# Kernel optimization log

Measured on AMD Instinct MI355X. Metric: run time of the kernel, lower is better.

## Reference

```python
import jax, jax.numpy as jnp
import numpy as np

N_HEADS = 16
MAX_LEN = 4096
D_MODEL = 1024
EPS = 1e-6


def setup_inputs() -> dict:
    key = jax.random.key(0)
    ks = jax.random.split(key, 12)
    B, L, D = 4, 4096, D_MODEL
    s = 1.0 / np.sqrt(D)
    inp = {
        "q": jax.random.normal(ks[0], (B, L, D), jnp.float32),
        "k": jax.random.normal(ks[1], (B, L, D), jnp.float32),
        "v": jax.random.normal(ks[2], (B, L, D), jnp.float32),
        "Wq": jax.random.normal(ks[3], (D, D), jnp.float32) * s,
        "bq": jax.random.normal(ks[4], (D,), jnp.float32) * s,
        "Wk": jax.random.normal(ks[5], (D, D), jnp.float32) * s,
        "bk": jax.random.normal(ks[6], (D,), jnp.float32) * s,
        "Wv": jax.random.normal(ks[7], (D, D), jnp.float32) * s,
        "bv": jax.random.normal(ks[8], (D,), jnp.float32) * s,
        "Wo": jax.random.normal(ks[9], (D, D), jnp.float32) * s,
        "bo": jax.random.normal(ks[10], (D,), jnp.float32) * s,
    }
    return inp


def _cos_attn(q, k, v, Wq, bq, Wk, bk, Wv, bv, Wo, bo):
    B, Lq, D = q.shape
    Lk = k.shape[1]
    H = N_HEADS
    hd = D // H
    # torch Linear: x @ W^T + b
    qh = (q @ Wq.T + bq).reshape(B, Lq, H, hd).transpose(0, 2, 1, 3)  # b h l d
    kh = (k @ Wk.T + bk).reshape(B, Lk, H, hd).transpose(0, 2, 1, 3)
    vh = (v @ Wv.T + bv).reshape(B, Lk, H, hd).transpose(0, 2, 1, 3)
    qh = jax.nn.relu(qh)
    kh = jax.nn.relu(kh)
    # weight_index buffer: pi*(1..max_len)/(2*max_len), shape (1,1,L,1)
    idx = (np.pi * jnp.arange(1, MAX_LEN + 1, dtype=jnp.float32) / (2 * MAX_LEN))
    qi = idx[:Lq][None, None, :, None]
    ki = idx[:Lk][None, None, :, None]
    q_ = jnp.concatenate([qh * jnp.sin(qi), qh * jnp.cos(qi)], axis=-1)  # b h l 2d
    k_ = jnp.concatenate([kh * jnp.sin(ki), kh * jnp.cos(ki)], axis=-1)
    kv_ = jnp.einsum("bnld,bnlm->bndm", k_, vh)  # b h 2d d
    z_ = 1.0 / jnp.maximum(jnp.einsum("bnld,bnd->bnl", q_, jnp.sum(k_, axis=2)), EPS)
    attn = jnp.einsum("bnld,bndm,bnl->bnlm", q_, kv_, z_)  # b h l d
    attn = attn.transpose(0, 2, 1, 3).reshape(B, Lq, D)
    return attn @ Wo.T + bo  # dropout: eval mode (identity)


def reference(q, k, v, Wq, bq, Wk, bk, Wv, bv, Wo, bo):
    return _cos_attn(q, k, v, Wq, bq, Wk, bk, Wv, bv, Wo, bo)
```

## Files before the change

kernel.cpp:

```cpp
#include <hip/hip_runtime.h>

typedef __bf16 bf16x8 __attribute__((ext_vector_type(8)));
typedef float f32x4 __attribute__((ext_vector_type(4)));

#define PI_F 3.14159265358979323846f

__device__ __forceinline__ unsigned short f2bf(float f) {
  unsigned u = __builtin_bit_cast(unsigned, f);
  u += 0x7fffu + ((u >> 16) & 1u);
  return (unsigned short)(u >> 16);
}

__device__ __forceinline__ unsigned scale_pair(unsigned w, float f) {
  const float lo = __builtin_bit_cast(float, w << 16);
  const float hi = __builtin_bit_cast(float, w & 0xffff0000u);
  return (unsigned)f2bf(lo * f) | ((unsigned)f2bf(hi * f) << 16);
}

#define GLD16(gp, lp)                                          \
  __builtin_amdgcn_global_load_lds(                            \
      (const __attribute__((address_space(1))) void*)(gp),     \
      (__attribute__((address_space(3))) void*)(lp), 16, 0, 0)

struct AReg { float4 a0, a1, a2, a3, a4, a5, a6, a7; };

__device__ __forceinline__ uint4 cvtpk16(float4 x, float4 y) {
  unsigned c0, c1, c2, c3;
  asm("v_cvt_pk_bf16_f32 %0, %1, %2" : "=v"(c0) : "v"(x.x), "v"(x.y));
  asm("v_cvt_pk_bf16_f32 %0, %1, %2" : "=v"(c1) : "v"(x.z), "v"(x.w));
  asm("v_cvt_pk_bf16_f32 %0, %1, %2" : "=v"(c2) : "v"(y.x), "v"(y.y));
  asm("v_cvt_pk_bf16_f32 %0, %1, %2" : "=v"(c3) : "v"(y.z), "v"(y.w));
  uint4 u; u.x = c0; u.y = c1; u.z = c2; u.w = c3;
  return u;
}

__device__ __forceinline__ uint2 cvtpk8(float a, float b, float c, float d) {
  unsigned lo, hi;
  asm("v_cvt_pk_bf16_f32 %0, %1, %2" : "=v"(lo) : "v"(a), "v"(b));
  asm("v_cvt_pk_bf16_f32 %0, %1, %2" : "=v"(hi) : "v"(c), "v"(d));
  uint2 r; r.x = lo; r.y = hi;
  return r;
}

__device__ __forceinline__ void unpack8(uint4 w, float* f) {
  f[0] = __builtin_bit_cast(float, w.x << 16);
  f[1] = __builtin_bit_cast(float, w.x & 0xffff0000u);
  f[2] = __builtin_bit_cast(float, w.y << 16);
  f[3] = __builtin_bit_cast(float, w.y & 0xffff0000u);
  f[4] = __builtin_bit_cast(float, w.z << 16);
  f[5] = __builtin_bit_cast(float, w.z & 0xffff0000u);
  f[6] = __builtin_bit_cast(float, w.w << 16);
  f[7] = __builtin_bit_cast(float, w.w & 0xffff0000u);
}

__global__ __launch_bounds__(256) void convert_w(
    const float* __restrict__ Wq, const float* __restrict__ Wk,
    const float* __restrict__ Wv, const float* __restrict__ Wo,
    unsigned short* __restrict__ Wqb, unsigned short* __restrict__ Wkb,
    unsigned short* __restrict__ Wvb, unsigned short* __restrict__ Wob) {
  const int region = blockIdx.y;
  const float* s; unsigned short* d;
  switch (region) {
    case 0: s = Wq; d = Wqb; break;
    case 1: s = Wk; d = Wkb; break;
    case 2: s = Wv; d = Wvb; break;
    default: s = Wo; d = Wob; break;
  }
  const float4* s4 = (const float4*)s;
  ushort4* d4 = (ushort4*)d;
  const int n4 = 262144;
  for (int i = blockIdx.x * 256 + threadIdx.x; i < n4; i += gridDim.x * 256) {
    float4 f = s4[i];
    ushort4 o;
    o.x = f2bf(f.x); o.y = f2bf(f.y); o.z = f2bf(f.z); o.w = f2bf(f.w);
    d4[i] = o;
  }
}

template <int MODE>
__global__ __launch_bounds__(512, 2) void gemm256(
    const float* __restrict__ A32, const unsigned short* __restrict__ Bw,
    const float* __restrict__ bias, unsigned short* __restrict__ out) {
  constexpr int K = 1024, NKT = 16;
  __shared__ unsigned short S[65536];
  const int tid = threadIdx.x;
  const int wave = tid >> 6, lane = tid & 63;
  const int fr = lane & 15, fq = lane >> 4;
  const int wr = wave >> 2, wc = wave & 3;
  const int cpx = gridDim.x >> 3;
  const int wg = (blockIdx.x & 7) * cpx + (blockIdx.x >> 3);
  const int mt = wg >> 2, ntile = wg & 3;
  const int m0 = mt * 256, n0 = ntile * 256;

  const int srow = tid >> 3;
  const int ac16 = tid & 7;
  const int scolE = ((ac16 << 4) ^ ((srow & 7) << 4)) >> 1;
  const unsigned short* bSrc = Bw + (size_t)(n0 + srow) * K + scolE;
  const int awoff = (ac16 ^ (srow & 7)) << 3;
  AReg R;

#define BSTAGE(kt_, buf_) do {                                                     \
    const int kc_ = (kt_) * 64;                                                    \
    GLD16(bSrc + kc_,                  S + (buf_) * 32768 + 16384 + wave * 512);   \
    GLD16(bSrc + (size_t)65536 + kc_,  S + (buf_) * 32768 + 20480 + wave * 512);   \
    GLD16(bSrc + (size_t)131072 + kc_, S + (buf_) * 32768 + 24576 + wave * 512);   \
    GLD16(bSrc + (size_t)196608 + kc_, S + (buf_) * 32768 + 28672 + wave * 512);   \
  } while (0)

#define ALOAD_ALL(kt_) do {                                                        \
    const int kc_ = (kt_) * 64;                                                    \
    const float4* p_;                                                              \
    p_ = (const float4*)(A32 + (size_t)(m0 + srow) * K + kc_) + ac16 * 2;          \
    R.a0 = p_[0]; R.a1 = p_[1];                                                    \
    p_ = (const float4*)(A32 + (size_t)(m0 + 64 + srow) * K + kc_) + ac16 * 2;     \
    R.a2 = p_[0]; R.a3 = p_[1];                                                    \
    p_ = (const float4*)(A32 + (size_t)(m0 + 128 + srow) * K + kc_) + ac16 * 2;    \
    R.a4 = p_[0]; R.a5 = p_[1];                                                    \
    p_ = (const float4*)(A32 + (size_t)(m0 + 192 + srow) * K + kc_) + ac16 * 2;    \
    R.a6 = p_[0]; R.a7 = p_[1];                                                    \
  } while (0)

#define AWRITE_ALL(buf_) do {                                                      \
    unsigned short* dst_ = &S[(buf_) * 32768 + srow * 64 + awoff];                 \
    *(uint4*)(dst_)         = cvtpk16(R.a0, R.a1);                                 \
    *(uint4*)(dst_ + 4096)  = cvtpk16(R.a2, R.a3);                                 \
    *(uint4*)(dst_ + 8192)  = cvtpk16(R.a4, R.a5);                                 \
    *(uint4*)(dst_ + 12288) = cvtpk16(R.a6, R.a7);                                 \
  } while (0)

  const int xorv = (fr & 7) << 4;
  const unsigned cbE0 = (unsigned)(((fq * 16) ^ xorv) >> 1);
  const unsigned cbE1 = (unsigned)(((64 + fq * 16) ^ xorv) >> 1);

  f32x4 acc[8][4] = {};
  ALOAD_ALL(0);
  BSTAGE(0, 0);
  AWRITE_ALL(0);
  asm volatile("s_waitcnt vmcnt(0) lgkmcnt(0)" ::: "memory");
  __syncthreads();

  for (int kt = 0; kt < NKT; ++kt) {
    const int buf = kt & 1;
    const unsigned aB = (unsigned)(buf * 32768 + wr * 8192 + fr * 64);
    const unsigned bB = (unsigned)(buf * 32768 + 16384 + (wc >> 1) * 8192 +
                                   ((wc & 1) * 64 + fr) * 64);
    bf16x8 af[4][2], b0[2][2], b1[2][2];
#pragma unroll
    for (int mm = 0; mm < 4; ++mm) {
      const unsigned r = aB + (unsigned)(mm * 1024);
      af[mm][0] = *(const bf16x8*)&S[r + cbE0];
      af[mm][1] = *(const bf16x8*)&S[r + cbE1];
    }
#pragma unroll
    for (int nn = 0; nn < 2; ++nn) {
      const unsigned r0 = bB + (unsigned)(nn * 1024);
      b0[nn][0] = *(const bf16x8*)&S[r0 + cbE0];
      b0[nn][1] = *(const bf16x8*)&S[r0 + cbE1];
      const unsigned r1 = bB + (unsigned)((2 + nn) * 1024);
      b1[nn][0] = *(const bf16x8*)&S[r1 + cbE0];
      b1[nn][1] = *(const bf16x8*)&S[r1 + cbE1];
    }
    if (kt + 1 < NKT) {
      ALOAD_ALL(kt + 1);
      BSTAGE(kt + 1, buf ^ 1);
    }
    __builtin_amdgcn_s_barrier();
    __builtin_amdgcn_s_setprio(1);
#pragma unroll
    for (int mm = 0; mm < 4; ++mm) {
#pragma unroll
      for (int nn = 0; nn < 2; ++nn) {
        acc[mm][nn] = __builtin_amdgcn_mfma_f32_16x16x32_bf16(af[mm][0], b0[nn][0], acc[mm][nn], 0, 0, 0);
        acc[mm][nn] = __builtin_amdgcn_mfma_f32_16x16x32_bf16(af[mm][1], b0[nn][1], acc[mm][nn], 0, 0, 0);
        acc[mm][2 + nn] = __builtin_amdgcn_mfma_f32_16x16x32_bf16(af[mm][0], b1[nn][0], acc[mm][2 + nn], 0, 0, 0);
        acc[mm][2 + nn] = __builtin_amdgcn_mfma_f32_16x16x32_bf16(af[mm][1], b1[nn][1], acc[mm][2 + nn], 0, 0, 0);
      }
    }
    __builtin_amdgcn_s_setprio(0);
    __builtin_amdgcn_s_barrier();
#pragma unroll
    for (int mm = 0; mm < 4; ++mm) {
      const unsigned r = aB + (unsigned)((4 + mm) * 1024);
      af[mm][0] = *(const bf16x8*)&S[r + cbE0];
      af[mm][1] = *(const bf16x8*)&S[r + cbE1];
    }
    if (kt + 1 < NKT) AWRITE_ALL(buf ^ 1);
    __builtin_amdgcn_s_barrier();
    __builtin_amdgcn_s_setprio(1);
#pragma unroll
    for (int mm = 0; mm < 4; ++mm) {
#pragma unroll
      for (int nn = 0; nn < 2; ++nn) {
        acc[4 + mm][nn] = __builtin_amdgcn_mfma_f32_16x16x32_bf16(af[mm][0], b0[nn][0], acc[4 + mm][nn], 0, 0, 0);
        acc[4 + mm][nn] = __builtin_amdgcn_mfma_f32_16x16x32_bf16(af[mm][1], b0[nn][1], acc[4 + mm][nn], 0, 0, 0);
        acc[4 + mm][2 + nn] = __builtin_amdgcn_mfma_f32_16x16x32_bf16(af[mm][0], b1[nn][0], acc[4 + mm][2 + nn], 0, 0, 0);
        acc[4 + mm][2 + nn] = __builtin_amdgcn_mfma_f32_16x16x32_bf16(af[mm][1], b1[nn][1], acc[4 + mm][2 + nn], 0, 0, 0);
      }
    }
    __builtin_amdgcn_s_setprio(0);
    asm volatile("s_waitcnt vmcnt(0) lgkmcnt(0)" ::: "memory");
    __builtin_amdgcn_s_barrier();
  }
#undef BSTAGE
#undef ALOAD_ALL
#undef AWRITE_ALL

  const int colb = n0 + wc * 64 + fr;
  const int rtb0 = wr * 128 + fq * 4;
  const int mlo = m0 & 4095;
  const int b16 = (m0 >> 12) << 4;
  const int hbase = n0 >> 6;

  if constexpr (MODE == 0) {
    float bb4[4];
#pragma unroll
    for (int nq = 0; nq < 4; ++nq) bb4[nq] = bias[colb + nq * 16];
    __syncthreads();
#pragma unroll
    for (int mq = 0; mq < 8; ++mq) {
#pragma unroll
      for (int rr = 0; rr < 4; ++rr) {
        const int rt = rtb0 + mq * 16 + rr;
        const int e = (rt >> 2) & 7;
#pragma unroll
        for (int nq = 0; nq < 4; ++nq) {
          const int ct = wc * 64 + nq * 16 + fr;
          const int sct = (ct & 7) | ((((ct >> 3) ^ e) & 31) << 3);
          S[rt * 256 + sct] = f2bf(fmaxf(acc[mq][nq][rr] + bb4[nq], 0.0f));
        }
      }
    }
    __syncthreads();
#pragma unroll
    for (int it = 0; it < 16; ++it) {
      const int rt = it * 16 + (tid >> 5);
      const int co = tid & 31;
      const int chunk = co ^ ((rt >> 2) & 7);
      uint4 w = *(const uint4*)&S[rt * 256 + chunk * 8];
      const int h = hbase + (co >> 3);
      const size_t addr = ((size_t)(b16 + h) * 4096 + mlo + rt) * 64 + ((co & 7) << 3);
      *(uint4*)(out + addr) = w;
    }
  } else {
    float bb4[4];
#pragma unroll
    for (int nq = 0; nq < 4; ++nq) bb4[nq] = bias[colb + nq * 16];
#pragma unroll
    for (int mq = 0; mq < 8; ++mq)
#pragma unroll
      for (int nq = 0; nq < 4; ++nq)
#pragma unroll
        for (int rr = 0; rr < 4; ++rr) {
          float val = acc[mq][nq][rr] + bb4[nq];
          if constexpr (MODE == 5) val = fmaxf(val, 0.0f);
          acc[mq][nq][rr] = val;
        }
    __syncthreads();
#pragma unroll
    for (int mq = 0; mq < 8; ++mq) {
      const int rtb = rtb0 + mq * 16;
#pragma unroll
      for (int nq = 0; nq < 4; ++nq) {
        const int ct = wc * 64 + nq * 16 + fr;
        uint2 w = cvtpk8(acc[mq][nq][0], acc[mq][nq][1], acc[mq][nq][2], acc[mq][nq][3]);
        *(uint2*)&S[ct * 256 + (rtb ^ ((ct & 7) << 2))] = w;
      }
    }
    __syncthreads();
#pragma unroll
    for (int it = 0; it < 16; ++it) {
      const int ct = it * 16 + (tid >> 5);
      const int lo = (tid & 31) << 3;
      const int sw = (ct & 7) << 2;
      uint2 r0 = *(const uint2*)&S[ct * 256 + (lo ^ sw)];
      uint2 r1 = *(const uint2*)&S[ct * 256 + ((lo + 4) ^ sw)];
      uint4 w; w.x = r0.x; w.y = r0.y; w.z = r1.x; w.w = r1.y;
      const int h = hbase + (ct >> 6), dd = ct & 63;
      const size_t addr = ((size_t)(b16 + h) * 64 + dd) * 4096 + mlo + lo;
      *(uint4*)(out + addr) = w;
    }
  }
}

__global__ __launch_bounds__(512, 2) void gemm_o(
    const unsigned short* __restrict__ Ain, const unsigned short* __restrict__ Bw,
    const float* __restrict__ bias, unsigned short* __restrict__ out) {
  constexpr int K = 1024, NKT = 16;
  __shared__ unsigned short S[65536];
  const int tid = threadIdx.x;
  const int wave = tid >> 6, lane = tid & 63;
  const int fr = lane & 15, fq = lane >> 4;
  const int wr = wave >> 2, wc = wave & 3;
  const int wg = (blockIdx.x & 7) * 32 + (blockIdx.x >> 3);
  const int mt = wg >> 2, ntile = wg & 3;
  const int m0 = mt * 256, n0 = ntile * 256;

  const int srow = tid >> 3;
  const int ac16 = tid & 7;
  const int scolE = ((ac16 << 4) ^ ((srow & 7) << 4)) >> 1;
  const unsigned short* bSrc = Bw + (size_t)(n0 + srow) * K + scolE;
  const unsigned short* aSrcB = Ain + (size_t)(m0 + srow) * K + scolE;

#define BSTAGE(kt_, buf_) do {                                                     \
    const int kc_ = (kt_) * 64;                                                    \
    GLD16(bSrc + kc_,                  S + (buf_) * 32768 + 16384 + wave * 512);   \
    GLD16(bSrc + (size_t)65536 + kc_,  S + (buf_) * 32768 + 20480 + wave * 512);   \
    GLD16(bSrc + (size_t)131072 + kc_, S + (buf_) * 32768 + 24576 + wave * 512);   \
    GLD16(bSrc + (size_t)196608 + kc_, S + (buf_) * 32768 + 28672 + wave * 512);   \
  } while (0)

#define ASTAGE(kt_, buf_) do {                                                     \
    const int kc_ = (kt_) * 64;                                                    \
    GLD16(aSrcB + kc_,                  S + (buf_) * 32768 +     0 + wave * 512);  \
    GLD16(aSrcB + (size_t)65536 + kc_,  S + (buf_) * 32768 +  4096 + wave * 512);  \
    GLD16(aSrcB + (size_t)131072 + kc_, S + (buf_) * 32768 +  8192 + wave * 512);  \
    GLD16(aSrcB + (size_t)196608 + kc_, S + (buf_) * 32768 + 12288 + wave * 512);  \
  } while (0)

  const int xorv = (fr & 7) << 4;
  const unsigned cbE0 = (unsigned)(((fq * 16) ^ xorv) >> 1);
  const unsigned cbE1 = (unsigned)(((64 + fq * 16) ^ xorv) >> 1);

  f32x4 acc[8][4] = {};
  BSTAGE(0, 0);
  ASTAGE(0, 0);
  asm volatile("s_waitcnt vmcnt(0)" ::: "memory");
  __syncthreads();

  for (int kt = 0; kt < NKT; ++kt) {
    const int buf = kt & 1;
    const unsigned aB = (unsigned)(buf * 32768 + wr * 8192 + fr * 64);
    const unsigned bB = (unsigned)(buf * 32768 + 16384 + (wc >> 1) * 8192 +
                                   ((wc & 1) * 64 + fr) * 64);
    bf16x8 af[4][2], b0[2][2], b1[2][2];
#pragma unroll
    for (int mm = 0; mm < 4; ++mm) {
      const unsigned r = aB + (unsigned)(mm * 1024);
      af[mm][0] = *(const bf16x8*)&S[r + cbE0];
      af[mm][1] = *(const bf16x8*)&S[r + cbE1];
    }
#pragma unroll
    for (int nn = 0; nn < 2; ++nn) {
      const unsigned r0 = bB + (unsigned)(nn * 1024);
      b0[nn][0] = *(const bf16x8*)&S[r0 + cbE0];
      b0[nn][1] = *(const bf16x8*)&S[r0 + cbE1];
      const unsigned r1 = bB + (unsigned)((2 + nn) * 1024);
      b1[nn][0] = *(const bf16x8*)&S[r1 + cbE0];
      b1[nn][1] = *(const bf16x8*)&S[r1 + cbE1];
    }
    if (kt + 1 < NKT) {
      BSTAGE(kt + 1, buf ^ 1);
      ASTAGE(kt + 1, buf ^ 1);
    }
    __builtin_amdgcn_s_barrier();
    __builtin_amdgcn_s_setprio(1);
#pragma unroll
    for (int mm = 0; mm < 4; ++mm) {
#pragma unroll
      for (int nn = 0; nn < 2; ++nn) {
        acc[mm][nn] = __builtin_amdgcn_mfma_f32_16x16x32_bf16(af[mm][0], b0[nn][0], acc[mm][nn], 0, 0, 0);
        acc[mm][nn] = __builtin_amdgcn_mfma_f32_16x16x32_bf16(af[mm][1], b0[nn][1], acc[mm][nn], 0, 0, 0);
        acc[mm][2 + nn] = __builtin_amdgcn_mfma_f32_16x16x32_bf16(af[mm][0], b1[nn][0], acc[mm][2 + nn], 0, 0, 0);
        acc[mm][2 + nn] = __builtin_amdgcn_mfma_f32_16x16x32_bf16(af[mm][1], b1[nn][1], acc[mm][2 + nn], 0, 0, 0);
      }
    }
    __builtin_amdgcn_s_setprio(0);
    __builtin_amdgcn_s_barrier();
#pragma unroll
    for (int mm = 0; mm < 4; ++mm) {
      const unsigned r = aB + (unsigned)((4 + mm) * 1024);
      af[mm][0] = *(const bf16x8*)&S[r + cbE0];
      af[mm][1] = *(const bf16x8*)&S[r + cbE1];
    }
    __builtin_amdgcn_s_barrier();
    __builtin_amdgcn_s_setprio(1);
#pragma unroll
    for (int mm = 0; mm < 4; ++mm) {
#pragma unroll
      for (int nn = 0; nn < 2; ++nn) {
        acc[4 + mm][nn] = __builtin_amdgcn_mfma_f32_16x16x32_bf16(af[mm][0], b0[nn][0], acc[4 + mm][nn], 0, 0, 0);
        acc[4 + mm][nn] = __builtin_amdgcn_mfma_f32_16x16x32_bf16(af[mm][1], b0[nn][1], acc[4 + mm][nn], 0, 0, 0);
        acc[4 + mm][2 + nn] = __builtin_amdgcn_mfma_f32_16x16x32_bf16(af[mm][0], b1[nn][0], acc[4 + mm][2 + nn], 0, 0, 0);
        acc[4 + mm][2 + nn] = __builtin_amdgcn_mfma_f32_16x16x32_bf16(af[mm][1], b1[nn][1], acc[4 + mm][2 + nn], 0, 0, 0);
      }
    }
    __builtin_amdgcn_s_setprio(0);
    asm volatile("s_waitcnt vmcnt(0) lgkmcnt(0)" ::: "memory");
    __builtin_amdgcn_s_barrier();
  }
#undef BSTAGE
#undef ASTAGE

  const int colb = n0 + wc * 64 + fr;
  float* Sf = (float*)S;
  float bb4[4];
#pragma unroll
  for (int nq = 0; nq < 4; ++nq) bb4[nq] = bias[colb + nq * 16];
  const int colL = wc * 64;
#pragma unroll
  for (int h4 = 0; h4 < 4; ++h4) {
    __syncthreads();
    if (wr == (h4 >> 1)) {
      const int mqb = (h4 & 1) * 4;
#pragma unroll
      for (int mq2 = 0; mq2 < 4; ++mq2) {
        const int rl = mq2 * 16 + fq * 4;
#pragma unroll
        for (int nq = 0; nq < 4; ++nq) {
#pragma unroll
          for (int rr = 0; rr < 4; ++rr)
            Sf[(rl + rr) * 260 + colL + nq * 16 + fr] = acc[mqb + mq2][nq][rr] + bb4[nq];
        }
      }
    }
    __syncthreads();
#pragma unroll
    for (int i = 0; i < 8; ++i) {
      const int rl = wave * 8 + i;
      const int gr = m0 + h4 * 64 + rl;
      f32x4 v4 = *(const f32x4*)&Sf[rl * 260 + lane * 4];
      uint2 w = cvtpk8(v4.x, v4.y, v4.z, v4.w);
      *(uint2*)(out + (size_t)gr * 1024 + n0 + lane * 4) = w;
    }
  }
}

__global__ __launch_bounds__(256) void expand_bf16_f32(
    const unsigned short* __restrict__ in, float* __restrict__ out) {
  const int stride = gridDim.x * 256;
  for (int i = blockIdx.x * 256 + threadIdx.x; i < 4194304; i += stride) {
    uint2 w = ((const uint2*)in)[i];
    f32x4 o;
    o.x = __builtin_bit_cast(float, w.x << 16);
    o.y = __builtin_bit_cast(float, w.x & 0xffff0000u);
    o.z = __builtin_bit_cast(float, w.y << 16);
    o.w = __builtin_bit_cast(float, w.y & 0xffff0000u);
    ((f32x4*)out)[i] = o;
  }
}

__global__ __launch_bounds__(256, 2) void kv_gemm(
    const unsigned short* __restrict__ Vt,
    const unsigned short* __restrict__ Kt,
    float* __restrict__ kvp) {
  __shared__ unsigned short As[64 * 64];
  __shared__ unsigned short Bs[128 * 64];
  __shared__ float sn[512], cn[512];
  const int tid = threadIdx.x, wave = tid >> 6, lane = tid & 63;
  const int fr = lane & 15, fq = lane >> 4;
  const int ls = blockIdx.x, bh = blockIdx.y;
  const size_t base = (size_t)bh * 64 * 4096;
  {
    float s0, c0, s1, c1;
    __sincosf(PI_F * (float)(ls * 512 + tid + 1) * (1.0f / 8192.0f), &s0, &c0);
    __sincosf(PI_F * (float)(ls * 512 + tid + 257) * (1.0f / 8192.0f), &s1, &c1);
    sn[tid] = s0; cn[tid] = c0;
    sn[tid + 256] = s1; cn[tid + 256] = c1;
  }
  f32x4 acc[5][2] = {};
  bf16x8 ones;
#pragma unroll
  for (int j = 0; j < 8; ++j) ones[j] = (__bf16)1.0f;
  for (int t = 0; t < 8; ++t) {
    const int l0 = ls * 512 + t * 64;
    __syncthreads();
#pragma unroll
    for (int j = 0; j < 2; ++j) {
      const int p = j * 256 + tid;
      const int row = p >> 3, cc = (p & 7) ^ (row & 7);
      GLD16(Vt + base + (size_t)row * 4096 + l0 + cc * 8,
            As + ((j << 8) + (wave << 6)) * 8);
    }
#pragma unroll
    for (int j = 0; j < 2; ++j) {
      const int p = j * 256 + tid;
      const int kr = p >> 3, cc = p & 7;
      const uint4 w = *(const uint4*)(Kt + base + (size_t)kr * 4096 + l0 + cc * 8);
      const int tl = t * 64 + cc * 8;
      float kf[8];
      unpack8(w, kf);
      const float4 sA = *(const float4*)&sn[tl], sB = *(const float4*)&sn[tl + 4];
      const float4 cA = *(const float4*)&cn[tl], cB = *(const float4*)&cn[tl + 4];
      float4 x0, x1;
      x0.x = kf[0] * sA.x; x0.y = kf[1] * sA.y; x0.z = kf[2] * sA.z; x0.w = kf[3] * sA.w;
      x1.x = kf[4] * sB.x; x1.y = kf[5] * sB.y; x1.z = kf[6] * sB.z; x1.w = kf[7] * sB.w;
      const uint4 wsn = cvtpk16(x0, x1);
      x0.x = kf[0] * cA.x; x0.y = kf[1] * cA.y; x0.z = kf[2] * cA.z; x0.w = kf[3] * cA.w;
      x1.x = kf[4] * cB.x; x1.y = kf[5] * cB.y; x1.z = kf[6] * cB.z; x1.w = kf[7] * cB.w;
      const uint4 wcn = cvtpk16(x0, x1);
      const int sw_ = cc ^ (kr & 7);
      *(uint4*)&Bs[(kr * 8 + sw_) * 8] = wsn;
      *(uint4*)&Bs[((kr + 64) * 8 + sw_) * 8] = wcn;
    }
    __syncthreads();
#pragma unroll
    for (int kk = 0; kk < 2; ++kk) {
      const int ch = kk * 4 + fq;
      bf16x8 a[4], b[2];
#pragma unroll
      for (int m = 0; m < 4; ++m) {
        const int r = m * 16 + fr;
        a[m] = *(const bf16x8*)&As[(r * 8 + (ch ^ (r & 7))) * 8];
      }
#pragma unroll
      for (int n = 0; n < 2; ++n) {
        const int r = wave * 32 + n * 16 + fr;
        b[n] = *(const bf16x8*)&Bs[(r * 8 + (ch ^ (r & 7))) * 8];
      }
#pragma unroll
      for (int m = 0; m < 4; ++m)
#pragma unroll
        for (int n = 0; n < 2; ++n)
          acc[m][n] = __builtin_amdgcn_mfma_f32_16x16x32_bf16(a[m], b[n], acc[m][n], 0, 0, 0);
#pragma unroll
      for (int n = 0; n < 2; ++n)
        acc[4][n] = __builtin_amdgcn_mfma_f32_16x16x32_bf16(ones, b[n], acc[4][n], 0, 0, 0);
    }
  }
  float* outp = kvp + ((size_t)bh * 8 + ls) * (65 * 128);
  const int colb = wave * 32 + fr;
#pragma unroll
  for (int n = 0; n < 2; ++n) {
    const int col = colb + n * 16;
#pragma unroll
    for (int m = 0; m < 4; ++m)
#pragma unroll
      for (int r = 0; r < 4; ++r)
        outp[(m * 16 + fq * 4 + r) * 128 + col] = acc[m][n][r];
    if (fq == 0) outp[64 * 128 + col] = acc[4][n][0];
  }
}

__global__ __launch_bounds__(256) void kv_reduce(
    const float* __restrict__ kvp, unsigned short* __restrict__ kv_ext) {
  const int bh = blockIdx.x;
  for (int e = threadIdx.x; e < 80 * 128; e += 256) {
    const int row = e >> 7, c = e & 127;
    float v = 0.0f;
    if (row < 65) {
#pragma unroll
      for (int ls = 0; ls < 8; ++ls)
        v += kvp[((size_t)bh * 8 + ls) * (65 * 128) + row * 128 + c];
    }
    kv_ext[(size_t)bh * (80 * 128) + e] = f2bf(v);
  }
}

__global__ __launch_bounds__(256) void attn_phase2(
    const unsigned short* __restrict__ Qh, const unsigned short* __restrict__ kve,
    unsigned short* __restrict__ attn) {
  __shared__ unsigned short Qs[128 * 128];
  __shared__ unsigned short Ws[80 * 128];
  const int tid = threadIdx.x, wave = tid >> 6, lane = tid & 63;
  const int fr = lane & 15, fq = lane >> 4;
  const int l0 = blockIdx.x * 128;
  const int bh = blockIdx.y, b = bh >> 4, h = bh & 15;
#pragma unroll
  for (int j = 0; j < 5; ++j) {
    const int p = j * 256 + tid;
    const int r = p >> 4, scn = p & 15;
    const int cc = scn ^ (r & 7);
    GLD16(kve + ((size_t)bh * 80 + r) * 128 + cc * 8,
          Ws + ((size_t)(j * 256 + wave * 64)) * 8);
  }
#pragma unroll
  for (int it = 0; it < 4; ++it) {
    const int qc = it * 256 + tid;
    const int r = qc >> 3, dc = qc & 7;
    const uint4 w = *(const uint4*)(Qh + ((size_t)bh * 4096 + l0 + r) * 64 + dc * 8);
    float sv, cv;
    __sincosf(PI_F * (float)(l0 + r + 1) * (1.0f / 8192.0f), &sv, &cv);
    uint4 osn, ocs;
    osn.x = scale_pair(w.x, sv); osn.y = scale_pair(w.y, sv);
    osn.z = scale_pair(w.z, sv); osn.w = scale_pair(w.w, sv);
    ocs.x = scale_pair(w.x, cv); ocs.y = scale_pair(w.y, cv);
    ocs.z = scale_pair(w.z, cv); ocs.w = scale_pair(w.w, cv);
    const int ps = r * 16 + (dc ^ (r & 7));
    *(uint4*)&Qs[ps * 8] = osn;
    *(uint4*)&Qs[(ps + 8) * 8] = ocs;
  }
  __syncthreads();
  f32x4 acc[2][5] = {};
#pragma unroll
  for (int kk = 0; kk < 4; ++kk) {
    const int cc = kk * 4 + fq;
    bf16x8 a[2], bb[5];
#pragma unroll
    for (int m = 0; m < 2; ++m) {
      const int r = wave * 32 + m * 16 + fr;
      a[m] = *(const bf16x8*)&Qs[(r * 16 + (cc ^ (r & 7))) * 8];
    }
#pragma unroll
    for (int n = 0; n < 5; ++n) {
      const int r = n * 16 + fr;
      bb[n] = *(const bf16x8*)&Ws[(r * 16 + (cc ^ (r & 7))) * 8];
    }
#pragma unroll
    for (int m = 0; m < 2; ++m)
#pragma unroll
      for (int n = 0; n < 5; ++n)
        acc[m][n] = __builtin_amdgcn_mfma_f32_16x16x32_bf16(a[m], bb[n], acc[m][n], 0, 0, 0);
  }
#pragma unroll
  for (int m = 0; m < 2; ++m) {
#pragma unroll
    for (int r = 0; r < 4; ++r) {
      const float den = __shfl(acc[m][4][r], lane & 48);
      const float z = 1.0f / fmaxf(den, 1e-6f);
      const int l = l0 + wave * 32 + m * 16 + fq * 4 + r;
      const size_t ro = ((size_t)b * 4096 + l) * 1024 + (size_t)h * 64;
#pragma unroll
      for (int n = 0; n < 4; ++n)
        attn[ro + n * 16 + fr] = f2bf(acc[m][n][r] * z);
    }
  }
}

extern "C" void kernel_launch(void* const* d_in, const int* in_sizes, int n_in,
                              void* d_out, int out_size, void* d_ws, size_t ws_size,
                              hipStream_t stream) {
  (void)in_sizes; (void)n_in; (void)out_size; (void)ws_size;
  const float* q  = (const float*)d_in[0];
  const float* k  = (const float*)d_in[1];
  const float* v  = (const float*)d_in[2];
  const float* Wq = (const float*)d_in[3];
  const float* bq = (const float*)d_in[4];
  const float* Wk = (const float*)d_in[5];
  const float* bk = (const float*)d_in[6];
  const float* Wv = (const float*)d_in[7];
  const float* bvp = (const float*)d_in[8];
  const float* Wo = (const float*)d_in[9];
  const float* bo = (const float*)d_in[10];

  char* ws = (char*)d_ws;
  unsigned short* Wqb = (unsigned short*)(ws + 0);
  unsigned short* Wkb = (unsigned short*)(ws + 2097152);
  unsigned short* Wvb = (unsigned short*)(ws + 4194304);
  unsigned short* Wob = (unsigned short*)(ws + 6291456);
  unsigned short* Qh  = (unsigned short*)(ws + 8388608);
  unsigned short* Vt  = (unsigned short*)(ws + 41943040);
  unsigned short* Kt  = (unsigned short*)(ws + 75497472);
  unsigned short* attnb = Kt;
  unsigned short* obf = Qh;
  float* kvp          = (float*)(ws + 109051904);
  unsigned short* kve = (unsigned short*)(ws + 126091264);

  convert_w<<<dim3(128, 4), 256, 0, stream>>>(Wq, Wk, Wv, Wo, Wqb, Wkb, Wvb, Wob);
  gemm256<0><<<256, 512, 0, stream>>>(q, Wqb, bq, Qh);
  gemm256<5><<<256, 512, 0, stream>>>(k, Wkb, bk, Kt);
  gemm256<4><<<256, 512, 0, stream>>>(v, Wvb, bvp, Vt);
  kv_gemm<<<dim3(8, 64), 256, 0, stream>>>(Vt, Kt, kvp);
  kv_reduce<<<64, 256, 0, stream>>>(kvp, kve);
  attn_phase2<<<dim3(32, 64), 256, 0, stream>>>(Qh, kve, attnb);
  gemm_o<<<256, 512, 0, stream>>>(attnb, Wob, bo, obf);
  expand_bf16_f32<<<2048, 256, 0, stream>>>(obf, (float*)d_out);
}
```

Measured before the change: 271.2 us.

## Deepen GEMM prefetch to two k-tiles with triple-buffered B in LDS

Both projection GEMM kernels now prefetch the weight (B) tile two k-steps ahead, using three rotating LDS buffers, and wait with a partial vmcnt instead of draining all outstanding loads each iteration. In the fp32-A kernel, a second register set holds the next-next A tile so the global loads for A are also issued two steps early. The aim is to hide more global-memory latency behind the MFMA work. In exchange, LDS per block grows to 160KB and register pressure rises, which could cause spills. The hand-written vmcnt counts must also match the issued loads exactly for correctness.

```diff
diff --git a/kernel.cpp b/kernel.cpp
--- a/kernel.cpp
+++ b/kernel.cpp
@@ -82,7 +82,7 @@
     const float* __restrict__ A32, const unsigned short* __restrict__ Bw,
     const float* __restrict__ bias, unsigned short* __restrict__ out) {
   constexpr int K = 1024, NKT = 16;
-  __shared__ unsigned short S[65536];
+  __shared__ unsigned short S[81920];
   const int tid = threadIdx.x;
   const int wave = tid >> 6, lane = tid & 63;
   const int fr = lane & 15, fq = lane >> 4;
@@ -97,35 +97,36 @@
   const int scolE = ((ac16 << 4) ^ ((srow & 7) << 4)) >> 1;
   const unsigned short* bSrc = Bw + (size_t)(n0 + srow) * K + scolE;
   const int awoff = (ac16 ^ (srow & 7)) << 3;
-  AReg R;
-
-#define BSTAGE(kt_, buf_) do {                                                     \
+  AReg R0, R1;
+
+#define BSTAGE(kt_, idx_) do {                                                     \
     const int kc_ = (kt_) * 64;                                                    \
-    GLD16(bSrc + kc_,                  S + (buf_) * 32768 + 16384 + wave * 512);   \
-    GLD16(bSrc + (size_t)65536 + kc_,  S + (buf_) * 32768 + 20480 + wave * 512);   \
-    GLD16(bSrc + (size_t)131072 + kc_, S + (buf_) * 32768 + 24576 + wave * 512);   \
-    GLD16(bSrc + (size_t)196608 + kc_, S + (buf_) * 32768 + 28672 + wave * 512);   \
+    unsigned short* bb_ = S + 32768 + (idx_) * 16384 + wave * 512;                 \
+    GLD16(bSrc + kc_, bb_);                                                        \
+    GLD16(bSrc + (size_t)65536 + kc_, bb_ + 4096);                                 \
+    GLD16(bSrc + (size_t)131072 + kc_, bb_ + 8192);                                \
+    GLD16(bSrc + (size_t)196608 + kc_, bb_ + 12288);                               \
   } while (0)
 
-#define ALOAD_ALL(kt_) do {                                                        \
+#define ALOAD_ALL(kt_, RR) do {                                                    \
     const int kc_ = (kt_) * 64;                                                    \
     const float4* p_;                                                              \
     p_ = (const float4*)(A32 + (size_t)(m0 + srow) * K + kc_) + ac16 * 2;          \
-    R.a0 = p_[0]; R.a1 = p_[1];                                                    \
+    RR.a0 = p_[0]; RR.a1 = p_[1];                                                  \
     p_ = (const float4*)(A32 + (size_t)(m0 + 64 + srow) * K + kc_) + ac16 * 2;     \
-    R.a2 = p_[0]; R.a3 = p_[1];                                                    \
+    RR.a2 = p_[0]; RR.a3 = p_[1];                                                  \
     p_ = (const float4*)(A32 + (size_t)(m0 + 128 + srow) * K + kc_) + ac16 * 2;    \
-    R.a4 = p_[0]; R.a5 = p_[1];                                                    \
+    RR.a4 = p_[0]; RR.a5 = p_[1];                                                  \
     p_ = (const float4*)(A32 + (size_t)(m0 + 192 + srow) * K + kc_) + ac16 * 2;    \
-    R.a6 = p_[0]; R.a7 = p_[1];                                                    \
+    RR.a6 = p_[0]; RR.a7 = p_[1];                                                  \
   } while (0)
 
-#define AWRITE_ALL(buf_) do {                                                      \
-    unsigned short* dst_ = &S[(buf_) * 32768 + srow * 64 + awoff];                 \
-    *(uint4*)(dst_)         = cvtpk16(R.a0, R.a1);                                 \
-    *(uint4*)(dst_ + 4096)  = cvtpk16(R.a2, R.a3);                                 \
-    *(uint4*)(dst_ + 8192)  = cvtpk16(R.a4, R.a5);                                 \
-    *(uint4*)(dst_ + 12288) = cvtpk16(R.a6, R.a7);                                 \
+#define AWRITE_ALL(idx_, RR) do {                                                  \
+    unsigned short* dst_ = &S[(idx_) * 16384 + srow * 64 + awoff];                 \
+    *(uint4*)(dst_)         = cvtpk16(RR.a0, RR.a1);                               \
+    *(uint4*)(dst_ + 4096)  = cvtpk16(RR.a2, RR.a3);                               \
+    *(uint4*)(dst_ + 8192)  = cvtpk16(RR.a4, RR.a5);                               \
+    *(uint4*)(dst_ + 12288) = cvtpk16(RR.a6, RR.a7);                               \
   } while (0)
 
   const int xorv = (fr & 7) << 4;
@@ -133,16 +134,18 @@
   const unsigned cbE1 = (unsigned)(((64 + fq * 16) ^ xorv) >> 1);
 
   f32x4 acc[8][4] = {};
-  ALOAD_ALL(0);
+  ALOAD_ALL(0, R0);
   BSTAGE(0, 0);
-  AWRITE_ALL(0);
-  asm volatile("s_waitcnt vmcnt(0) lgkmcnt(0)" ::: "memory");
-  __syncthreads();
-
+  ALOAD_ALL(1, R1);
+  BSTAGE(1, 1);
+  AWRITE_ALL(0, R0);
+  asm volatile("s_waitcnt vmcnt(12) lgkmcnt(0)" ::: "memory");
+  __builtin_amdgcn_s_barrier();
+
+  int bcur = 0;
   for (int kt = 0; kt < NKT; ++kt) {
-    const int buf = kt & 1;
-    const unsigned aB = (unsigned)(buf * 32768 + wr * 8192 + fr * 64);
-    const unsigned bB = (unsigned)(buf * 32768 + 16384 + (wc >> 1) * 8192 +
+    const unsigned aB = (unsigned)((kt & 1) * 16384 + wr * 8192 + fr * 64);
+    const unsigned bB = (unsigned)(32768 + bcur * 16384 + (wc >> 1) * 8192 +
                                    ((wc & 1) * 64 + fr) * 64);
     bf16x8 af[4][2], b0[2][2], b1[2][2];
 #pragma unroll
@@ -160,9 +163,10 @@
       b1[nn][0] = *(const bf16x8*)&S[r1 + cbE0];
       b1[nn][1] = *(const bf16x8*)&S[r1 + cbE1];
     }
-    if (kt + 1 < NKT) {
-      ALOAD_ALL(kt + 1);
-      BSTAGE(kt + 1, buf ^ 1);
+    if (kt + 2 < NKT) {
+      int bst = bcur + 2; if (bst >= 3) bst -= 3;
+      if ((kt & 1) == 0) { ALOAD_ALL(kt + 2, R0); } else { ALOAD_ALL(kt + 2, R1); }
+      BSTAGE(kt + 2, bst);
     }
     __builtin_amdgcn_s_barrier();
     __builtin_amdgcn_s_setprio(1);
@@ -184,7 +188,9 @@
       af[mm][0] = *(const bf16x8*)&S[r + cbE0];
       af[mm][1] = *(const bf16x8*)&S[r + cbE1];
     }
-    if (kt + 1 < NKT) AWRITE_ALL(buf ^ 1);
+    if (kt + 1 < NKT) {
+      if ((kt & 1) == 0) { AWRITE_ALL((kt + 1) & 1, R1); } else { AWRITE_ALL((kt + 1) & 1, R0); }
+    }
     __builtin_amdgcn_s_barrier();
     __builtin_amdgcn_s_setprio(1);
 #pragma unroll
@@ -198,8 +204,13 @@
       }
     }
     __builtin_amdgcn_s_setprio(0);
-    asm volatile("s_waitcnt vmcnt(0) lgkmcnt(0)" ::: "memory");
-    __builtin_amdgcn_s_barrier();
+    if (kt + 2 < NKT) {
+      asm volatile("s_waitcnt vmcnt(12) lgkmcnt(0)" ::: "memory");
+    } else {
+      asm volatile("s_waitcnt vmcnt(0) lgkmcnt(0)" ::: "memory");
+    }
+    __builtin_amdgcn_s_barrier();
+    bcur = bcur + 1; if (bcur == 3) bcur = 0;
   }
 #undef BSTAGE
 #undef ALOAD_ALL
@@ -286,7 +297,7 @@
     const unsigned short* __restrict__ Ain, const unsigned short* __restrict__ Bw,
     const float* __restrict__ bias, unsigned short* __restrict__ out) {
   constexpr int K = 1024, NKT = 16;
-  __shared__ unsigned short S[65536];
+  __shared__ unsigned short S[81920];
   const int tid = threadIdx.x;
   const int wave = tid >> 6, lane = tid & 63;
   const int fr = lane & 15, fq = lane >> 4;
@@ -301,20 +312,22 @@
   const unsigned short* bSrc = Bw + (size_t)(n0 + srow) * K + scolE;
   const unsigned short* aSrcB = Ain + (size_t)(m0 + srow) * K + scolE;
 
-#define BSTAGE(kt_, buf_) do {                                                     \
+#define BSTAGE(kt_, idx_) do {                                                     \
     const int kc_ = (kt_) * 64;                                                    \
-    GLD16(bSrc + kc_,                  S + (buf_) * 32768 + 16384 + wave * 512);   \
-    GLD16(bSrc + (size_t)65536 + kc_,  S + (buf_) * 32768 + 20480 + wave * 512);   \
-    GLD16(bSrc + (size_t)131072 + kc_, S + (buf_) * 32768 + 24576 + wave * 512);   \
-    GLD16(bSrc + (size_t)196608 + kc_, S + (buf_) * 32768 + 28672 + wave * 512);   \
+    unsigned short* bb_ = S + 32768 + (idx_) * 16384 + wave * 512;                 \
+    GLD16(bSrc + kc_, bb_);                                                        \
+    GLD16(bSrc + (size_t)65536 + kc_, bb_ + 4096);                                 \
+    GLD16(bSrc + (size_t)131072 + kc_, bb_ + 8192);                                \
+    GLD16(bSrc + (size_t)196608 + kc_, bb_ + 12288);                               \
   } while (0)
 
-#define ASTAGE(kt_, buf_) do {                                                     \
+#define ASTAGE(kt_, idx_) do {                                                     \
     const int kc_ = (kt_) * 64;                                                    \
-    GLD16(aSrcB + kc_,                  S + (buf_) * 32768 +     0 + wave * 512);  \
-    GLD16(aSrcB + (size_t)65536 + kc_,  S + (buf_) * 32768 +  4096 + wave * 512);  \
-    GLD16(aSrcB + (size_t)131072 + kc_, S + (buf_) * 32768 +  8192 + wave * 512);  \
-    GLD16(aSrcB + (size_t)196608 + kc_, S + (buf_) * 32768 + 12288 + wave * 512);  \
+    unsigned short* ab_ = S + (idx_) * 16384 + wave * 512;                         \
+    GLD16(aSrcB + kc_, ab_);                                                       \
+    GLD16(aSrcB + (size_t)65536 + kc_, ab_ + 4096);                                \
+    GLD16(aSrcB + (size_t)131072 + kc_, ab_ + 8192);                               \
+    GLD16(aSrcB + (size_t)196608 + kc_, ab_ + 12288);                              \
   } while (0)
 
   const int xorv = (fr & 7) << 4;
@@ -322,15 +335,16 @@
   const unsigned cbE1 = (unsigned)(((64 + fq * 16) ^ xorv) >> 1);
 
   f32x4 acc[8][4] = {};
+  ASTAGE(0, 0);
   BSTAGE(0, 0);
-  ASTAGE(0, 0);
-  asm volatile("s_waitcnt vmcnt(0)" ::: "memory");
-  __syncthreads();
-
+  BSTAGE(1, 1);
+  asm volatile("s_waitcnt vmcnt(4)" ::: "memory");
+  __builtin_amdgcn_s_barrier();
+
+  int bcur = 0;
   for (int kt = 0; kt < NKT; ++kt) {
-    const int buf = kt & 1;
-    const unsigned aB = (unsigned)(buf * 32768 + wr * 8192 + fr * 64);
-    const unsigned bB = (unsigned)(buf * 32768 + 16384 + (wc >> 1) * 8192 +
+    const unsigned aB = (unsigned)((kt & 1) * 16384 + wr * 8192 + fr * 64);
+    const unsigned bB = (unsigned)(32768 + bcur * 16384 + (wc >> 1) * 8192 +
                                    ((wc & 1) * 64 + fr) * 64);
     bf16x8 af[4][2], b0[2][2], b1[2][2];
 #pragma unroll
@@ -348,9 +362,10 @@
       b1[nn][0] = *(const bf16x8*)&S[r1 + cbE0];
       b1[nn][1] = *(const bf16x8*)&S[r1 + cbE1];
     }
-    if (kt + 1 < NKT) {
-      BSTAGE(kt + 1, buf ^ 1);
-      ASTAGE(kt + 1, buf ^ 1);
+    if (kt + 1 < NKT) ASTAGE(kt + 1, (kt + 1) & 1);
+    if (kt + 2 < NKT) {
+      int bst = bcur + 2; if (bst >= 3) bst -= 3;
+      BSTAGE(kt + 2, bst);
     }
     __builtin_amdgcn_s_barrier();
     __builtin_amdgcn_s_setprio(1);
@@ -385,8 +400,13 @@
       }
     }
     __builtin_amdgcn_s_setprio(0);
-    asm volatile("s_waitcnt vmcnt(0) lgkmcnt(0)" ::: "memory");
-    __builtin_amdgcn_s_barrier();
+    if (kt + 2 < NKT) {
+      asm volatile("s_waitcnt vmcnt(4) lgkmcnt(0)" ::: "memory");
+    } else {
+      asm volatile("s_waitcnt vmcnt(0) lgkmcnt(0)" ::: "memory");
+    }
+    __builtin_amdgcn_s_barrier();
+    bcur = bcur + 1; if (bcur == 3) bcur = 0;
   }
 #undef BSTAGE
 #undef ASTAGE
```

After: 748.7 us. 2.76x slower.
